# Kernel tuning notes

Measured on AMD Instinct MI355X. Metric: run time of the kernel, lower is better.

The kernel has to match this reference:

```python
import jax, jax.numpy as jnp
import numpy as np

NUM_EMBEDDINGS = 1024
EMBEDDING_DIM = 256
SPLIT = 8
SPLIT_DIM = EMBEDDING_DIM // SPLIT  # 32
COMMITMENT_COST = 0.25
DECAY = 0.99
EPSILON = 1e-05


def setup_inputs() -> dict:
    key = jax.random.key(0)
    k1, k2, k3 = jax.random.split(key, 3)
    inputs = jax.random.normal(k1, (16384, EMBEDDING_DIM), dtype=jnp.float32)
    embedding = jax.random.normal(k2, (NUM_EMBEDDINGS, SPLIT_DIM), dtype=jnp.float32)
    ema_cluster_size = jnp.zeros((NUM_EMBEDDINGS,), dtype=jnp.float32)
    ema_w = jax.random.normal(k3, (NUM_EMBEDDINGS, SPLIT_DIM), dtype=jnp.float32)
    return {"inputs": inputs, "embedding": embedding,
            "ema_cluster_size": ema_cluster_size, "ema_w": ema_w}


def reference(inputs, embedding, ema_cluster_size, ema_w):
    B = inputs.shape[0]
    flat = inputs.reshape(-1, SPLIT_DIM)  # [B*split, d]
    rows = flat.shape[0]

    # squared euclidean distances to codebook: [rows, K]
    distances = (jnp.sum(flat ** 2, axis=1, keepdims=True)
                 + jnp.sum(embedding ** 2, axis=1)
                 - 2.0 * flat @ embedding.T)
    idx = jnp.argmin(distances, axis=1)  # [rows]

    # one-hot @ embedding == gather (same math, efficient form)
    quantized_flat = embedding[idx]  # [rows, d]

    # EMA statistics (training-mode update); quantization uses the OLD weights,
    # exactly as in the torch forward.
    counts = jax.ops.segment_sum(jnp.ones((rows,), jnp.float32), idx,
                                 num_segments=NUM_EMBEDDINGS)
    dw = jax.ops.segment_sum(flat, idx, num_segments=NUM_EMBEDDINGS)  # enc.T @ flat
    new_cs = ema_cluster_size * DECAY + (1.0 - DECAY) * counts
    n = jnp.sum(new_cs)
    new_cs = (new_cs + EPSILON) / (n + NUM_EMBEDDINGS * EPSILON) * n
    new_ema_w = ema_w * DECAY + (1.0 - DECAY) * dw
    new_embedding = new_ema_w / new_cs[:, None]

    # losses (EMA variant: only commitment term)
    e_latent_loss = jnp.mean((jax.lax.stop_gradient(quantized_flat) - flat) ** 2)
    loss = COMMITMENT_COST * e_latent_loss

    # straight-through estimator
    quantized_flat = flat + jax.lax.stop_gradient(quantized_flat - flat)
    quantized = quantized_flat.reshape(B, -1)  # [B, EMBEDDING_DIM]

    avg_probs = counts / rows  # mean of one-hot encodings over rows
    perplexity = jnp.exp(-jnp.sum(avg_probs * jnp.log(avg_probs + 1e-10)))

    encoding_indices = idx.reshape(B, SPLIT)
    return (loss, quantized, perplexity, encoding_indices,
            new_embedding, new_cs, new_ema_w)
```

## Files before the change

### kernel.cpp

```cpp
#include <hip/hip_runtime.h>

#define NUM_CODES 1024
#define DIM 32
#define ROWS 131072
#define DECAYF 0.99f
#define EPSF 1e-5f
#define CCOST 0.25f
#define SLAB 33792
#define RGROUPS 8
#define IBLK (SLAB / 256)
#define TILES_PER_CHUNK 16
#define DBIAS 256.0f

typedef __attribute__((ext_vector_type(8))) short short8v;
typedef __attribute__((ext_vector_type(4))) float f32x4;

__device__ __forceinline__ unsigned short bf16_rne(float f) {
    unsigned u = __float_as_uint(f);
    unsigned r = u + 0x7FFFu + ((u >> 16) & 1u);
    return (unsigned short)(r >> 16);
}

__global__ __launch_bounds__(256) void k_prep(const float* __restrict__ emb,
                                              unsigned short* __restrict__ bhi,
                                              unsigned short* __restrict__ blo,
                                              float* __restrict__ nbias,
                                              float* __restrict__ loss_sum) {
    int s = blockIdx.x * 256 + threadIdx.x;
    if (s == 0) loss_sum[0] = 0.0f;
    if (s < NUM_CODES) {
        const float4* e4 = (const float4*)(emb + s * DIM);
        float sum = 0.0f;
#pragma unroll
        for (int j = 0; j < 8; ++j) {
            float4 e = e4[j];
            sum += e.x * e.x + e.y * e.y + e.z * e.z + e.w * e.w;
        }
        nbias[s] = -0.5f * sum - DBIAS;
    }
    int l = s & 63, t = s >> 6;
    int code = t * 16 + (l & 15);
    int koff = (l >> 4) * 8;
    const float* src = emb + code * DIM + koff;
    float4 f0 = *(const float4*)(src);
    float4 f1 = *(const float4*)(src + 4);
    float fv[8] = {f0.x, f0.y, f0.z, f0.w, f1.x, f1.y, f1.z, f1.w};
    short8v h, lo;
#pragma unroll
    for (int j = 0; j < 8; ++j) {
        unsigned short hb = bf16_rne(fv[j]);
        float hf = __uint_as_float((unsigned)hb << 16);
        h[j]  = (short)hb;
        lo[j] = (short)bf16_rne(fv[j] - hf);
    }
    *(short8v*)(bhi + (size_t)s * 8) = h;
    *(short8v*)(blo + (size_t)s * 8) = lo;
}

__global__ __launch_bounds__(256) void k_argmin(const float* __restrict__ flat,
                                                const unsigned short* __restrict__ bhi_g,
                                                const unsigned short* __restrict__ blo_g,
                                                const float* __restrict__ nbias,
                                                unsigned* __restrict__ part) {
    const int lane = threadIdx.x & 63;
    const int wid  = threadIdx.x >> 6;
    const int rowbase = blockIdx.x * 32;
    const int lr = lane & 15;
    const int lg = lane >> 4;

    short8v ahi[2], alo[2];
#pragma unroll
    for (int rf = 0; rf < 2; ++rf) {
        const float* src = flat + (size_t)(rowbase + rf * 16 + lr) * DIM + lg * 8;
        float4 f0 = *(const float4*)src;
        float4 f1 = *(const float4*)(src + 4);
        float fv[8] = {f0.x, f0.y, f0.z, f0.w, f1.x, f1.y, f1.z, f1.w};
        short8v h, lo;
#pragma unroll
        for (int j = 0; j < 8; ++j) {
            unsigned short hb = bf16_rne(fv[j]);
            float hf = __uint_as_float((unsigned)hb << 16);
            h[j]  = (short)hb;
            lo[j] = (short)bf16_rne(fv[j] - hf);
        }
        ahi[rf] = h; alo[rf] = lo;
    }

    unsigned best[2][4];
#pragma unroll
    for (int rf = 0; rf < 2; ++rf)
#pragma unroll
        for (int rg = 0; rg < 4; ++rg) best[rf][rg] = 0xFFFFFFFFu;

    const int t0 = wid * TILES_PER_CHUNK;
#pragma unroll 2
    for (int tt = 0; tt < TILES_PER_CHUNK; ++tt) {
        const int t = t0 + tt;
        short8v bh = *(const short8v*)(bhi_g + ((size_t)t * 64 + lane) * 8);
        short8v bl = *(const short8v*)(blo_g + ((size_t)t * 64 + lane) * 8);
        float nn = nbias[t * 16 + lr];
        unsigned code = (unsigned)(t * 16 + lr);
#pragma unroll
        for (int rf = 0; rf < 2; ++rf) {
            f32x4 acc = {nn, nn, nn, nn};
            acc = __builtin_amdgcn_mfma_f32_16x16x32_bf16(ahi[rf], bh, acc, 0, 0, 0);
            acc = __builtin_amdgcn_mfma_f32_16x16x32_bf16(ahi[rf], bl, acc, 0, 0, 0);
            acc = __builtin_amdgcn_mfma_f32_16x16x32_bf16(alo[rf], bh, acc, 0, 0, 0);
#pragma unroll
            for (int rg = 0; rg < 4; ++rg) {
                unsigned pb = (__float_as_uint(acc[rg]) & 0xFFFFFC00u) | code;
                best[rf][rg] = min(best[rf][rg], pb);
            }
        }
    }

#pragma unroll
    for (int rf = 0; rf < 2; ++rf) {
#pragma unroll
        for (int rg = 0; rg < 4; ++rg) {
            unsigned b = best[rf][rg];
#pragma unroll
            for (int m = 1; m < 16; m <<= 1)
                b = min(b, (unsigned)__shfl_xor((int)b, m));
            if (lr == rg)
                part[(size_t)wid * ROWS + rowbase + rf * 16 + lg * 4 + rg] = b;
        }
    }
}

__global__ __launch_bounds__(256) void k_scatter(const float* __restrict__ flat,
                                                 const float* __restrict__ emb,
                                                 const unsigned* __restrict__ part,
                                                 float* __restrict__ qout,
                                                 float* __restrict__ idxf_out,
                                                 float* __restrict__ slabs,
                                                 float* __restrict__ loss_sum,
                                                 int rows_per_block) {
    __shared__ float acc[SLAB];
    __shared__ float red[256];
    const int tid = threadIdx.x;
    for (int i = tid; i < SLAB; i += 256) acc[i] = 0.0f;
    __syncthreads();

    const int row0 = blockIdx.x * rows_per_block;
    float l = 0.0f;
    for (int rr = 0; rr < rows_per_block; rr += 256) {
        int r = row0 + rr + tid;
        unsigned p0 = part[r];
        unsigned p1 = part[(size_t)ROWS + r];
        unsigned p2 = part[2 * (size_t)ROWS + r];
        unsigned p3 = part[3 * (size_t)ROWS + r];
        unsigned pm = min(min(p0, p1), min(p2, p3));
        int k = (int)(pm & 1023u);
        idxf_out[r] = (float)k;

        const float4* f4 = (const float4*)(flat + (size_t)r * DIM);
        const float4* e4 = (const float4*)(emb + (size_t)k * DIM);
        float4* q4 = (float4*)(qout + (size_t)r * DIM);
        int kb = k * DIM;
#pragma unroll
        for (int j4 = 0; j4 < 8; ++j4) {
            float4 f = f4[j4];
            float4 e = e4[j4];
            q4[j4] = e;
            float dx = e.x - f.x, dy = e.y - f.y, dz = e.z - f.z, dv = e.w - f.w;
            l += dx * dx + dy * dy + dz * dz + dv * dv;
            int j = 4 * j4;
            atomicAdd(&acc[kb + ((j + 0 + k) & 31)], f.x);
            atomicAdd(&acc[kb + ((j + 1 + k) & 31)], f.y);
            atomicAdd(&acc[kb + ((j + 2 + k) & 31)], f.z);
            atomicAdd(&acc[kb + ((j + 3 + k) & 31)], f.w);
        }
        atomicAdd(&acc[32768 + k], 1.0f);
    }
    __syncthreads();

    float* slab = slabs + (size_t)blockIdx.x * SLAB;
    for (int i = tid; i < 32768; i += 256) {
        int k = i >> 5, j = i & 31;
        slab[i] = acc[(i & ~31) | ((j + k) & 31)];
    }
    for (int i = tid; i < NUM_CODES; i += 256) slab[32768 + i] = acc[32768 + i];

    red[tid] = l;
    __syncthreads();
    for (int s = 128; s > 0; s >>= 1) {
        if (tid < s) red[tid] += red[tid + s];
        __syncthreads();
    }
    if (tid == 0) atomicAdd(loss_sum, red[0]);
}

__global__ __launch_bounds__(256) void k_reduce1(const float* __restrict__ slabs,
                                                 float* __restrict__ partial,
                                                 int pcount) {
    int g  = blockIdx.x / IBLK;
    int ib = blockIdx.x % IBLK;
    int i = ib * 256 + threadIdx.x;
    const float* base = slabs + (size_t)g * pcount * SLAB + i;
    float s = 0.0f;
#pragma unroll 4
    for (int p = 0; p < pcount; ++p) s += base[(size_t)p * SLAB];
    partial[(size_t)g * SLAB + i] = s;
}

__global__ __launch_bounds__(256) void k_reduce2(const float* __restrict__ partial,
                                                 float* __restrict__ dw_sum,
                                                 float* __restrict__ counts_sum) {
    int i = blockIdx.x * 256 + threadIdx.x;
    float s = 0.0f;
#pragma unroll
    for (int g = 0; g < RGROUPS; ++g) s += partial[(size_t)g * SLAB + i];
    if (i < 32768) dw_sum[i] = s;
    else           counts_sum[i - 32768] = s;
}

__global__ __launch_bounds__(1024) void k_final(const float* __restrict__ ema_cs,
                                                const float* __restrict__ ema_w,
                                                const float* __restrict__ counts,
                                                const float* __restrict__ dw,
                                                const float* __restrict__ loss_sum,
                                                float* __restrict__ out_loss,
                                                float* __restrict__ out_perp,
                                                float* __restrict__ out_emb,
                                                float* __restrict__ out_cs,
                                                float* __restrict__ out_ema_w) {
    int tid = threadIdx.x;
    __shared__ float s_cs[NUM_CODES];
    __shared__ float red[1024];

    float c = counts[tid];
    float pre = ema_cs[tid] * DECAYF + (1.0f - DECAYF) * c;

    red[tid] = pre;
    __syncthreads();
    for (int s = 512; s > 0; s >>= 1) {
        if (tid < s) red[tid] += red[tid + s];
        __syncthreads();
    }
    float n = red[0];
    __syncthreads();

    float ncs = (pre + EPSF) / (n + (float)NUM_CODES * EPSF) * n;
    s_cs[tid] = ncs;
    out_cs[tid] = ncs;

    float p = c / (float)ROWS;
    red[tid] = p * logf(p + 1e-10f);
    __syncthreads();
    for (int s = 512; s > 0; s >>= 1) {
        if (tid < s) red[tid] += red[tid + s];
        __syncthreads();
    }
    if (tid == 0) {
        out_perp[0] = expf(-red[0]);
        out_loss[0] = CCOST * (loss_sum[0] / (float)((size_t)ROWS * DIM));
    }
    __syncthreads();

    for (int i = tid; i < NUM_CODES * DIM; i += 1024) {
        int k = i >> 5;
        float w = ema_w[i] * DECAYF + (1.0f - DECAYF) * dw[i];
        out_ema_w[i] = w;
        out_emb[i] = w / s_cs[k];
    }
}

extern "C" void kernel_launch(void* const* d_in, const int* in_sizes, int n_in,
                              void* d_out, int out_size, void* d_ws, size_t ws_size,
                              hipStream_t stream) {
    const float* inputs    = (const float*)d_in[0];
    const float* embedding = (const float*)d_in[1];
    const float* ema_cs    = (const float*)d_in[2];
    const float* ema_w     = (const float*)d_in[3];

    float* out        = (float*)d_out;
    float* out_loss   = out;
    float* out_q      = out + 1;
    float* out_perp   = out + 4194305;
    float* out_idxf   = out + 4194306;
    float* out_emb    = out + 4325378;
    float* out_cs     = out + 4358146;
    float* out_ema_w  = out + 4359170;

    char* ws = (char*)d_ws;
    float* nbias      = (float*)(ws);
    float* loss_sum   = (float*)(ws + 4096);
    float* counts_sum = (float*)(ws + 8192);
    float* dw_sum     = (float*)(ws + 12288);
    unsigned short* bhi_g = (unsigned short*)(ws + 143360);
    unsigned short* blo_g = (unsigned short*)(ws + 208896);
    unsigned* part    = (unsigned*)(ws + 274432);
    float* partial    = (float*)(ws + 2371584);
    float* slabs      = (float*)(ws + 3452928);

    size_t slab_off = 3452928;
    size_t avail = (ws_size > slab_off) ? (ws_size - slab_off) : 0;
    int P = 16;
    if (avail >= (size_t)256 * SLAB * 4) P = 256;
    else if (avail >= (size_t)128 * SLAB * 4) P = 128;
    else if (avail >= (size_t)64 * SLAB * 4) P = 64;
    else if (avail >= (size_t)32 * SLAB * 4) P = 32;
    int rows_per_block = ROWS / P;

    k_prep   <<<16, 256, 0, stream>>>(embedding, bhi_g, blo_g, nbias, loss_sum);
    k_argmin <<<ROWS / 32, 256, 0, stream>>>(inputs, bhi_g, blo_g, nbias, part);
    k_scatter<<<P, 256, 0, stream>>>(inputs, embedding, part, out_q, out_idxf,
                                     slabs, loss_sum, rows_per_block);
    k_reduce1<<<RGROUPS * IBLK, 256, 0, stream>>>(slabs, partial, P / RGROUPS);
    k_reduce2<<<IBLK, 256, 0, stream>>>(partial, dw_sum, counts_sum);
    k_final  <<<1, 1024, 0, stream>>>(ema_cs, ema_w, counts_sum, dw_sum, loss_sum,
                                      out_loss, out_perp, out_emb, out_cs, out_ema_w);
}
```

Measured before the change: 101.0 us.

## Fuse argmin finalization and gather into argmin kernel, compute loss algebraically

The argmin kernel now combines the per-wave partial minima in shared memory, then writes the index and the gathered quantized rows directly. This removes the global partial-index buffer and the gather from the scatter kernel. The commitment loss is rebuilt in the final kernel from sum(f^2) plus per-code terms (e^2*count - 2*e·dw), accumulated in double. The separate reduce2 kernel is dropped, with its group sum folded into k_final, and RGROUPS is halved. The trade-offs are more serial work in the single-block final kernel and possible precision differences in the loss.

Result: slower. 109.9 us (+8.9%).

```diff
diff --git a/kernel.cpp b/kernel.cpp
--- a/kernel.cpp
+++ b/kernel.cpp
@@ -7,7 +7,7 @@
 #define EPSF 1e-5f
 #define CCOST 0.25f
 #define SLAB 33792
-#define RGROUPS 8
+#define RGROUPS 4
 #define IBLK (SLAB / 256)
 #define TILES_PER_CHUNK 16
 #define DBIAS 256.0f
@@ -25,9 +25,9 @@
                                               unsigned short* __restrict__ bhi,
                                               unsigned short* __restrict__ blo,
                                               float* __restrict__ nbias,
-                                              float* __restrict__ loss_sum) {
+                                              float* __restrict__ sumf2) {
     int s = blockIdx.x * 256 + threadIdx.x;
-    if (s == 0) loss_sum[0] = 0.0f;
+    if (s == 0) sumf2[0] = 0.0f;
     if (s < NUM_CODES) {
         const float4* e4 = (const float4*)(emb + s * DIM);
         float sum = 0.0f;
@@ -61,7 +61,12 @@
                                                 const unsigned short* __restrict__ bhi_g,
                                                 const unsigned short* __restrict__ blo_g,
                                                 const float* __restrict__ nbias,
-                                                unsigned* __restrict__ part) {
+                                                const float* __restrict__ emb,
+                                                int* __restrict__ idx_out,
+                                                float* __restrict__ idxf_out,
+                                                float* __restrict__ qout) {
+    __shared__ unsigned win[4][32];
+    __shared__ int kwin[32];
     const int lane = threadIdx.x & 63;
     const int wid  = threadIdx.x >> 6;
     const int rowbase = blockIdx.x * 32;
@@ -122,19 +127,33 @@
 #pragma unroll
             for (int m = 1; m < 16; m <<= 1)
                 b = min(b, (unsigned)__shfl_xor((int)b, m));
-            if (lr == rg)
-                part[(size_t)wid * ROWS + rowbase + rf * 16 + lg * 4 + rg] = b;
-        }
+            if (lr == rg) win[wid][rf * 16 + lg * 4 + rg] = b;
+        }
+    }
+    __syncthreads();
+
+    if (threadIdx.x < 32) {
+        unsigned pm = min(min(win[0][threadIdx.x], win[1][threadIdx.x]),
+                          min(win[2][threadIdx.x], win[3][threadIdx.x]));
+        int k = (int)(pm & 1023u);
+        kwin[threadIdx.x] = k;
+        idx_out[rowbase + threadIdx.x]  = k;
+        idxf_out[rowbase + threadIdx.x] = (float)k;
+    }
+    __syncthreads();
+
+    {
+        int row = threadIdx.x >> 3, seg = threadIdx.x & 7;
+        int k = kwin[row];
+        float4 e = *(const float4*)(emb + (size_t)k * DIM + seg * 4);
+        *(float4*)(qout + (size_t)(rowbase + row) * DIM + seg * 4) = e;
     }
 }
 
 __global__ __launch_bounds__(256) void k_scatter(const float* __restrict__ flat,
-                                                 const float* __restrict__ emb,
-                                                 const unsigned* __restrict__ part,
-                                                 float* __restrict__ qout,
-                                                 float* __restrict__ idxf_out,
+                                                 const int* __restrict__ idx,
                                                  float* __restrict__ slabs,
-                                                 float* __restrict__ loss_sum,
+                                                 float* __restrict__ sumf2,
                                                  int rows_per_block) {
     __shared__ float acc[SLAB];
     __shared__ float red[256];
@@ -143,28 +162,16 @@
     __syncthreads();
 
     const int row0 = blockIdx.x * rows_per_block;
-    float l = 0.0f;
+    float sf = 0.0f;
     for (int rr = 0; rr < rows_per_block; rr += 256) {
         int r = row0 + rr + tid;
-        unsigned p0 = part[r];
-        unsigned p1 = part[(size_t)ROWS + r];
-        unsigned p2 = part[2 * (size_t)ROWS + r];
-        unsigned p3 = part[3 * (size_t)ROWS + r];
-        unsigned pm = min(min(p0, p1), min(p2, p3));
-        int k = (int)(pm & 1023u);
-        idxf_out[r] = (float)k;
-
+        int k = idx[r];
         const float4* f4 = (const float4*)(flat + (size_t)r * DIM);
-        const float4* e4 = (const float4*)(emb + (size_t)k * DIM);
-        float4* q4 = (float4*)(qout + (size_t)r * DIM);
         int kb = k * DIM;
 #pragma unroll
         for (int j4 = 0; j4 < 8; ++j4) {
             float4 f = f4[j4];
-            float4 e = e4[j4];
-            q4[j4] = e;
-            float dx = e.x - f.x, dy = e.y - f.y, dz = e.z - f.z, dv = e.w - f.w;
-            l += dx * dx + dy * dy + dz * dz + dv * dv;
+            sf += f.x * f.x + f.y * f.y + f.z * f.z + f.w * f.w;
             int j = 4 * j4;
             atomicAdd(&acc[kb + ((j + 0 + k) & 31)], f.x);
             atomicAdd(&acc[kb + ((j + 1 + k) & 31)], f.y);
@@ -182,13 +189,13 @@
     }
     for (int i = tid; i < NUM_CODES; i += 256) slab[32768 + i] = acc[32768 + i];
 
-    red[tid] = l;
+    red[tid] = sf;
     __syncthreads();
     for (int s = 128; s > 0; s >>= 1) {
         if (tid < s) red[tid] += red[tid + s];
         __syncthreads();
     }
-    if (tid == 0) atomicAdd(loss_sum, red[0]);
+    if (tid == 0) atomicAdd(sumf2, red[0]);
 }
 
 __global__ __launch_bounds__(256) void k_reduce1(const float* __restrict__ slabs,
@@ -204,22 +211,11 @@
     partial[(size_t)g * SLAB + i] = s;
 }
 
-__global__ __launch_bounds__(256) void k_reduce2(const float* __restrict__ partial,
-                                                 float* __restrict__ dw_sum,
-                                                 float* __restrict__ counts_sum) {
-    int i = blockIdx.x * 256 + threadIdx.x;
-    float s = 0.0f;
-#pragma unroll
-    for (int g = 0; g < RGROUPS; ++g) s += partial[(size_t)g * SLAB + i];
-    if (i < 32768) dw_sum[i] = s;
-    else           counts_sum[i - 32768] = s;
-}
-
 __global__ __launch_bounds__(1024) void k_final(const float* __restrict__ ema_cs,
                                                 const float* __restrict__ ema_w,
-                                                const float* __restrict__ counts,
-                                                const float* __restrict__ dw,
-                                                const float* __restrict__ loss_sum,
+                                                const float* __restrict__ emb,
+                                                const float* __restrict__ partial,
+                                                const float* __restrict__ sumf2,
                                                 float* __restrict__ out_loss,
                                                 float* __restrict__ out_perp,
                                                 float* __restrict__ out_emb,
@@ -227,9 +223,14 @@
                                                 float* __restrict__ out_ema_w) {
     int tid = threadIdx.x;
     __shared__ float s_cs[NUM_CODES];
+    __shared__ float s_cnt[NUM_CODES];
     __shared__ float red[1024];
-
-    float c = counts[tid];
+    __shared__ double redd[1024];
+
+    float c = 0.0f;
+#pragma unroll
+    for (int g = 0; g < RGROUPS; ++g) c += partial[(size_t)g * SLAB + 32768 + tid];
+    s_cnt[tid] = c;
     float pre = ema_cs[tid] * DECAYF + (1.0f - DECAYF) * c;
 
     red[tid] = pre;
@@ -252,17 +253,31 @@
         if (tid < s) red[tid] += red[tid + s];
         __syncthreads();
     }
-    if (tid == 0) {
-        out_perp[0] = expf(-red[0]);
-        out_loss[0] = CCOST * (loss_sum[0] / (float)((size_t)ROWS * DIM));
-    }
-    __syncthreads();
-
+    float nplogp = red[0];
+    __syncthreads();
+
+    double lterm = 0.0;
     for (int i = tid; i < NUM_CODES * DIM; i += 1024) {
         int k = i >> 5;
-        float w = ema_w[i] * DECAYF + (1.0f - DECAYF) * dw[i];
+        float dwv = 0.0f;
+#pragma unroll
+        for (int g = 0; g < RGROUPS; ++g) dwv += partial[(size_t)g * SLAB + i];
+        float e = emb[i];
+        lterm += (double)e * ((double)e * (double)s_cnt[k] - 2.0 * (double)dwv);
+        float w = ema_w[i] * DECAYF + (1.0f - DECAYF) * dwv;
         out_ema_w[i] = w;
         out_emb[i] = w / s_cs[k];
+    }
+    redd[tid] = lterm;
+    __syncthreads();
+    for (int s = 512; s > 0; s >>= 1) {
+        if (tid < s) redd[tid] += redd[tid + s];
+        __syncthreads();
+    }
+    if (tid == 0) {
+        double lsum = (double)sumf2[0] + redd[0];
+        out_loss[0] = (float)(CCOST * lsum / (double)((size_t)ROWS * DIM));
+        out_perp[0] = expf(-nplogp);
     }
 }
 
@@ -285,16 +300,14 @@
 
     char* ws = (char*)d_ws;
     float* nbias      = (float*)(ws);
-    float* loss_sum   = (float*)(ws + 4096);
-    float* counts_sum = (float*)(ws + 8192);
-    float* dw_sum     = (float*)(ws + 12288);
-    unsigned short* bhi_g = (unsigned short*)(ws + 143360);
-    unsigned short* blo_g = (unsigned short*)(ws + 208896);
-    unsigned* part    = (unsigned*)(ws + 274432);
-    float* partial    = (float*)(ws + 2371584);
-    float* slabs      = (float*)(ws + 3452928);
-
-    size_t slab_off = 3452928;
+    float* sumf2      = (float*)(ws + 4096);
+    int*   idx        = (int*)(ws + 8192);
+    unsigned short* bhi_g = (unsigned short*)(ws + 532480);
+    unsigned short* blo_g = (unsigned short*)(ws + 598016);
+    float* partial    = (float*)(ws + 663552);
+    float* slabs      = (float*)(ws + 1204224);
+
+    size_t slab_off = 1204224;
     size_t avail = (ws_size > slab_off) ? (ws_size - slab_off) : 0;
     int P = 16;
     if (avail >= (size_t)256 * SLAB * 4) P = 256;
@@ -303,12 +316,11 @@
     else if (avail >= (size_t)32 * SLAB * 4) P = 32;
     int rows_per_block = ROWS / P;
 
-    k_prep   <<<16, 256, 0, stream>>>(embedding, bhi_g, blo_g, nbias, loss_sum);
-    k_argmin <<<ROWS / 32, 256, 0, stream>>>(inputs, bhi_g, blo_g, nbias, part);
-    k_scatter<<<P, 256, 0, stream>>>(inputs, embedding, part, out_q, out_idxf,
-                                     slabs, loss_sum, rows_per_block);
+    k_prep   <<<16, 256, 0, stream>>>(embedding, bhi_g, blo_g, nbias, sumf2);
+    k_argmin <<<ROWS / 32, 256, 0, stream>>>(inputs, bhi_g, blo_g, nbias, embedding,
+                                             idx, out_idxf, out_q);
+    k_scatter<<<P, 256, 0, stream>>>(inputs, idx, slabs, sumf2, rows_per_block);
     k_reduce1<<<RGROUPS * IBLK, 256, 0, stream>>>(slabs, partial, P / RGROUPS);
-    k_reduce2<<<IBLK, 256, 0, stream>>>(partial, dw_sum, counts_sum);
-    k_final  <<<1, 1024, 0, stream>>>(ema_cs, ema_w, counts_sum, dw_sum, loss_sum,
+    k_final  <<<1, 1024, 0, stream>>>(ema_cs, ema_w, embedding, partial, sumf2,
                                       out_loss, out_perp, out_emb, out_cs, out_ema_w);
 }
```
